# Optimization experiments

Hardware: AMD Instinct MI355X
Metric: run time of the kernel (lower is better)

The kernel has to match this reference:

```python
import jax, jax.numpy as jnp
import numpy as np

# Model constants (from Equilibrium3BConfig + hardcoded MambaBlock args)
D_MODEL = 2560
D_INNER = 5120          # expand=2
N_STATE = 128           # d_state
HEADS = 80              # d_inner // headdim
P_HEAD = 64             # headdim
D_CONV = 4
CONV_DIM = D_INNER + 2 * N_STATE        # 5376 (x, B, C share the conv)
D_IN_PROJ = 2 * D_INNER + 2 * N_STATE + HEADS  # 10576 (z, xBC, dt)
N_EXPERTS = 16
TOP_K = 2
M_INTER = 864
MS_INTER = 1728
EPS = 1e-6


def _rms(x, w, eps=EPS):
    xf = x.astype(jnp.float32)
    xf = xf * jax.lax.rsqrt(jnp.mean(xf * xf, axis=-1, keepdims=True) + eps)
    return w * xf.astype(x.dtype)


def setup_inputs() -> dict:
    key = jax.random.key(0)
    ks = jax.random.split(key, 16)
    b, l = 1, 1024
    s = 0.02  # weight scale, keeps activations sane through the deep block
    return {
        "hidden_states": jax.random.normal(ks[0], (b, l, D_MODEL), jnp.float32),
        "w_in": jax.random.normal(ks[1], (D_MODEL, D_IN_PROJ), jnp.float32) * s,
        "conv_w": jax.random.normal(ks[2], (CONV_DIM, D_CONV), jnp.float32) * s,
        "conv_b": jnp.zeros((CONV_DIM,), jnp.float32),
        "dt_bias": jax.random.normal(ks[3], (HEADS,), jnp.float32) * s,
        "A_log": jax.random.normal(ks[4], (HEADS,), jnp.float32) * s,
        "D": jnp.ones((HEADS,), jnp.float32),
        "mamba_norm_w": jnp.ones((D_INNER,), jnp.float32),
        "w_out": jax.random.normal(ks[5], (D_INNER, D_MODEL), jnp.float32) * s,
        "ln1_w": jnp.ones((D_MODEL,), jnp.float32),
        "ln2_w": jnp.ones((D_MODEL,), jnp.float32),
        "router_w": jax.random.normal(ks[6], (D_MODEL, N_EXPERTS), jnp.float32) * s,
        "we_gate": jax.random.normal(ks[7], (N_EXPERTS, D_MODEL, M_INTER), jnp.float32) * s,
        "we_up": jax.random.normal(ks[8], (N_EXPERTS, D_MODEL, M_INTER), jnp.float32) * s,
        "we_down": jax.random.normal(ks[9], (N_EXPERTS, M_INTER, D_MODEL), jnp.float32) * s,
        "ws_gate": jax.random.normal(ks[10], (D_MODEL, MS_INTER), jnp.float32) * s,
        "ws_up": jax.random.normal(ks[11], (D_MODEL, MS_INTER), jnp.float32) * s,
        "ws_down": jax.random.normal(ks[12], (MS_INTER, D_MODEL), jnp.float32) * s,
    }


def _forward(hidden_states, w_in, conv_w, conv_b, dt_bias, A_log, D, mamba_norm_w,
             w_out, ln1_w, ln2_w, router_w, we_gate, we_up, we_down,
             ws_gate, ws_up, ws_down):
    b, l, d = hidden_states.shape

    # ---- Mamba2 (selective scan) sub-block ----
    residual = hidden_states
    x = _rms(hidden_states, ln1_w)
    zxbcdt = x @ w_in  # [b, l, 10576]
    z, xBC, dt = jnp.split(zxbcdt, [D_INNER, D_INNER + CONV_DIM], axis=-1)

    # depthwise causal conv over (x, B, C) channels, then SiLU
    xBC_t = xBC.transpose(0, 2, 1)  # [b, c, l]
    conv = jax.lax.conv_general_dilated(
        xBC_t, conv_w[:, None, :], (1,), [(D_CONV - 1, 0)],
        feature_group_count=CONV_DIM, dimension_numbers=("NCH", "OIH", "NCH"))
    xBC = jax.nn.silu((conv + conv_b[None, :, None]).transpose(0, 2, 1))
    xs, Bc, Cc = jnp.split(xBC, [D_INNER, D_INNER + N_STATE], axis=-1)

    dt = jax.nn.softplus(dt + dt_bias)          # [b, l, h]
    A = -jnp.exp(A_log)                          # [h]
    xh = xs.reshape(b, l, HEADS, P_HEAD)

    # time-major for scan
    dt_l = dt.transpose(1, 0, 2)                 # [l, b, h]
    xh_l = xh.transpose(1, 0, 2, 3)              # [l, b, h, p]
    B_l = Bc.transpose(1, 0, 2)                  # [l, b, n]
    C_l = Cc.transpose(1, 0, 2)                  # [l, b, n]

    def step(h, inp):
        dt_t, x_t, B_t, C_t = inp
        dA = jnp.exp(dt_t * A)                   # [b, h]
        h = h * dA[..., None, None] + (dt_t[..., None] * x_t)[..., None] * B_t[:, None, None, :]
        y = jnp.einsum("bhpn,bn->bhp", h, C_t)
        return h, y

    h0 = jnp.zeros((b, HEADS, P_HEAD, N_STATE), hidden_states.dtype)
    _, y_l = jax.lax.scan(step, h0, (dt_l, xh_l, B_l, C_l))
    y_l = y_l + D[None, None, :, None] * xh_l    # skip term
    y = y_l.transpose(1, 0, 2, 3).reshape(b, l, D_INNER)
    y = _rms(y * jax.nn.silu(z), mamba_norm_w)   # gated RMSNorm
    hidden = residual + y @ w_out

    # ---- DeepSeekMoE sub-block ----
    residual2 = hidden
    xm = _rms(hidden, ln2_w).reshape(b * l, d)
    logits = xm @ router_w
    probs = jax.nn.softmax(logits.astype(jnp.float32), axis=-1)
    topv, topi = jax.lax.top_k(probs, TOP_K)
    topv = topv / jnp.sum(topv, axis=-1, keepdims=True)  # renormalize top-k
    wdense = jnp.sum(jax.nn.one_hot(topi, N_EXPERTS, dtype=xm.dtype)
                     * topv[..., None].astype(xm.dtype), axis=1)  # [T, E]

    # routed experts (SwiGLU), dense-masked faithful math
    hexp = (jax.nn.silu(jnp.einsum("td,edm->tem", xm, we_gate))
            * jnp.einsum("td,edm->tem", xm, we_up))
    y_routed = jnp.einsum("tem,emd,te->td", hexp, we_down, wdense)

    # shared experts (single fused SwiGLU MLP)
    y_shared = (jax.nn.silu(xm @ ws_gate) * (xm @ ws_up)) @ ws_down

    moe = (y_routed + y_shared).reshape(b, l, d)
    return residual2 + moe


def reference(hidden_states, w_in, conv_w, conv_b, dt_bias, A_log, D, mamba_norm_w,
              w_out, ln1_w, ln2_w, router_w, we_gate, we_up, we_down,
              ws_gate, ws_up, ws_down):
    return _forward(hidden_states, w_in, conv_w, conv_b, dt_bias, A_log, D,
                    mamba_norm_w, w_out, ln1_w, ln2_w, router_w,
                    we_gate, we_up, we_down, ws_gate, ws_up, ws_down)
```

## Files before the change

### kernel.cpp

```cpp
#include <hip/hip_runtime.h>

typedef __attribute__((ext_vector_type(4))) float f32x4;
typedef __attribute__((ext_vector_type(8))) __bf16 bf16x8;
typedef __attribute__((ext_vector_type(4))) __bf16 bf16x4;
typedef __attribute__((ext_vector_type(8))) _Float16 f16x8;
typedef __attribute__((ext_vector_type(4))) _Float16 f16x4;

#define D_MODEL 2560
#define D_INNER 5120
#define N_STATE 128
#define HEADS 80
#define P_HEAD 64
#define CONV_DIM 5376
#define D_INPROJ 10576
#define SEQ 1024
#define NCHUNK 16
#define QCHUNK 64
#define NEXP 16
#define M_INTER 864
#define MS_INTER 1728
#define NSLOT 2048
#define NSLOTP 2176

__device__ __forceinline__ float siluf(float x) { return x / (1.f + __expf(-x)); }

__device__ __forceinline__ int swz_p(int k4, int P) {
  return (k4 & ~31) | ((((k4 >> 3) & 3) ^ P) << 3) | (k4 & 7);
}

__device__ __forceinline__ void gl16(const __bf16* g, __bf16* l) {
  __builtin_amdgcn_global_load_lds((const __attribute__((address_space(1))) unsigned int*)g,
                                   (__attribute__((address_space(3))) unsigned int*)l, 16, 0, 0);
}

__device__ __forceinline__ float block_sum256(float v, float* red) {
#pragma unroll
  for (int m = 32; m > 0; m >>= 1) v += __shfl_xor(v, m, 64);
  int w = threadIdx.x >> 6;
  if ((threadIdx.x & 63) == 0) red[w] = v;
  __syncthreads();
  return red[0] + red[1] + red[2] + red[3];
}

template <bool FP16>
__global__ __launch_bounds__(256) void k_rmsnorm_p(const float* __restrict__ in,
                                                   const float* __restrict__ w,
                                                   float* __restrict__ f32out,
                                                   __bf16* __restrict__ ph,
                                                   __bf16* __restrict__ pdh,
                                                   __bf16* __restrict__ pdl, int D) {
  __shared__ float red[4];
  int t = blockIdx.x, tid = threadIdx.x;
  const float* x = in + (size_t)t * D;
  int nd4 = D >> 2;
  float ss = 0.f;
  for (int i = tid; i < nd4; i += 256) {
    float4 v = ((const float4*)x)[i];
    ss += v.x * v.x + v.y * v.y + v.z * v.z + v.w * v.w;
  }
  float tot = block_sum256(ss, red);
  float r = rsqrtf(tot / (float)D + 1e-6f);
  int P = (t >> 1) & 3;
  for (int i = tid; i < nd4; i += 256) {
    float4 v = ((const float4*)x)[i];
    float4 wv = ((const float4*)w)[i];
    float4 o;
    o.x = wv.x * v.x * r; o.y = wv.y * v.y * r; o.z = wv.z * v.z * r; o.w = wv.w * v.w * r;
    if (f32out) ((float4*)(f32out + (size_t)t * D))[i] = o;
    int p = swz_p(i * 4, P);
    if constexpr (FP16) {
      f16x4 hv;
      hv[0] = (_Float16)o.x; hv[1] = (_Float16)o.y; hv[2] = (_Float16)o.z; hv[3] = (_Float16)o.w;
      *(f16x4*)&ph[(size_t)t * D + p] = hv;
    } else {
      bf16x4 hv;
      hv[0] = (__bf16)o.x; hv[1] = (__bf16)o.y; hv[2] = (__bf16)o.z; hv[3] = (__bf16)o.w;
      *(bf16x4*)&ph[(size_t)t * D + p] = hv;
    }
    if (pdh) {
      int pp = swz_p(i * 4, P);
      bf16x4 hv, lv;
      hv[0] = (__bf16)o.x; hv[1] = (__bf16)o.y; hv[2] = (__bf16)o.z; hv[3] = (__bf16)o.w;
      lv[0] = (__bf16)(o.x - (float)hv[0]); lv[1] = (__bf16)(o.y - (float)hv[1]);
      lv[2] = (__bf16)(o.z - (float)hv[2]); lv[3] = (__bf16)(o.w - (float)hv[3]);
      *(bf16x4*)&pdh[(size_t)t * D + pp] = hv;
      *(bf16x4*)&pdl[(size_t)t * D + pp] = lv;
    }
  }
}

__global__ __launch_bounds__(256) void k_redrms(const float* __restrict__ Pp,
                                                const float* __restrict__ res,
                                                float* __restrict__ hidden,
                                                const float* __restrict__ w,
                                                float* __restrict__ f32out,
                                                __bf16* __restrict__ ph) {
  __shared__ float vbuf[D_MODEL];
  __shared__ float red[4];
  int t = blockIdx.x, tid = threadIdx.x;
  const int n4 = D_MODEL / 4;
  float ss = 0.f;
  for (int i = tid; i < n4; i += 256) {
    f32x4 a = *(const f32x4*)&res[(size_t)t * D_MODEL + i * 4];
#pragma unroll
    for (int z = 0; z < 4; z++)
      a += *(const f32x4*)&Pp[(size_t)z * SEQ * D_MODEL + (size_t)t * D_MODEL + i * 4];
    *(f32x4*)&vbuf[i * 4] = a;
    *(f32x4*)&hidden[(size_t)t * D_MODEL + i * 4] = a;
    ss += a[0] * a[0] + a[1] * a[1] + a[2] * a[2] + a[3] * a[3];
  }
  float tot = block_sum256(ss, red);
  float r = rsqrtf(tot / (float)D_MODEL + 1e-6f);
  int P = (t >> 1) & 3;
  for (int i = tid; i < n4; i += 256) {
    f32x4 v = *(const f32x4*)&vbuf[i * 4];
    float4 wv = *(const float4*)&w[i * 4];
    f32x4 o;
    o[0] = wv.x * v[0] * r; o[1] = wv.y * v[1] * r; o[2] = wv.z * v[2] * r; o[3] = wv.w * v[3] * r;
    *(f32x4*)&f32out[(size_t)t * D_MODEL + i * 4] = o;
    int p = swz_p(i * 4, P);
    bf16x4 hv;
    hv[0] = (__bf16)o[0]; hv[1] = (__bf16)o[1]; hv[2] = (__bf16)o[2]; hv[3] = (__bf16)o[3];
    *(bf16x4*)&ph[(size_t)t * D_MODEL + p] = hv;
  }
}

template <bool SPLIT, bool FP16>
__global__ __launch_bounds__(256) void k_transW(const float* __restrict__ W, int ld, int K, int N,
                                                __bf16* __restrict__ Th, __bf16* __restrict__ Tl) {
  __shared__ float T[64][65];
  const int n0 = blockIdx.x * 64, k0 = blockIdx.y * 64, tid = threadIdx.x;
#pragma unroll
  for (int i = 0; i < 16; i++) {
    int idx = tid + i * 256;
    int k = idx >> 6, n = idx & 63;
    float v = 0.f;
    if (n0 + n < N) v = W[(size_t)(k0 + k) * ld + n0 + n];
    T[k][n] = v;
  }
  __syncthreads();
#pragma unroll
  for (int i = 0; i < 4; i++) {
    int idx = tid + i * 256;
    int n = idx >> 4, p4 = (idx & 15) * 4;
    int nn = n0 + n;
    int P = (nn >> 1) & 3;
    if constexpr (SPLIT) {
      bf16x4 hv, lv;
#pragma unroll
      for (int e = 0; e < 4; e++) {
        int p = p4 + e;
        int kk = swz_p(p, P);
        float v = T[kk][n];
        __bf16 h = (__bf16)v;
        hv[e] = h;
        lv[e] = (__bf16)(v - (float)h);
      }
      *(bf16x4*)&Th[(size_t)nn * K + k0 + p4] = hv;
      *(bf16x4*)&Tl[(size_t)nn * K + k0 + p4] = lv;
    } else if constexpr (FP16) {
      f16x4 hv;
#pragma unroll
      for (int e = 0; e < 4; e++) {
        int p = p4 + e;
        int kk = swz_p(p, P);
        hv[e] = (_Float16)T[kk][n];
      }
      *(f16x4*)&Th[(size_t)nn * K + k0 + p4] = hv;
    } else {
      bf16x4 hv;
#pragma unroll
      for (int e = 0; e < 4; e++) {
        int p = p4 + e;
        int kk = swz_p(p, P);
        hv[e] = (__bf16)T[kk][n];
      }
      *(bf16x4*)&Th[(size_t)nn * K + k0 + p4] = hv;
    }
  }
}

template <bool SPLIT, bool FP16, bool PIPE>
__global__ __launch_bounds__(256) void k_gemm2(const __bf16* __restrict__ Ah,
                                               const __bf16* __restrict__ Al,
                                               const __bf16* __restrict__ Bh,
                                               const __bf16* __restrict__ Bl,
                                               float* __restrict__ C,
                                               int M, int N, int K, int ks, int nst) {
  constexpr int PLE = 4096;
  constexpr int NPL = SPLIT ? 4 : 2;
  constexpr int NBUF = PIPE ? 2 : 1;
  __shared__ __bf16 lds[NBUF * NPL * PLE];

  const int tid = threadIdx.x;
  const int T = gridDim.x * gridDim.y * gridDim.z;
  const int linear = blockIdx.x + gridDim.x * (blockIdx.y + gridDim.y * blockIdx.z);
  const int s_idx = (linear & 7) * (T >> 3) + (linear >> 3);
  const int bm = s_idx & 7;
  const int g = s_idx >> 3;
  const int bn = g % gridDim.y;
  const int z = g / gridDim.y;

  const int m0 = bm * 128, n0 = bn * 128;
  const int s0 = (int)(((long long)z * nst) / ks);
  const int s1 = (int)(((long long)(z + 1) * nst) / ks);
  float* __restrict__ Cp = C + (size_t)z * M * N;

  const int lane = tid & 63, wid = tid >> 6;
  const int wr = wid >> 1, wc = wid & 1;
  const int l16 = lane & 15, kl = lane >> 4;

  const int srow = tid >> 2;
  const int schunk = (tid & 3) * 8;
  const size_t aB0 = (size_t)(m0 + srow) * K + schunk;
  const size_t aB1 = aB0 + (size_t)64 * K;
  const size_t bB0 = (size_t)(n0 + srow) * K + schunk;
  const size_t bB1 = bB0 + (size_t)64 * K;

  int aoff[4], boff[4];
#pragma unroll
  for (int mi = 0; mi < 4; mi++) {
    int ra = wr * 64 + mi * 16 + l16;
    int rb = wc * 64 + mi * 16 + l16;
    aoff[mi] = ra * 64 + ((kl ^ ((ra >> 1) & 3)) << 4);
    boff[mi] = rb * 64 + ((kl ^ ((rb >> 1) & 3)) << 4);
  }

  f32x4 acc[4][4];
#pragma unroll
  for (int mi = 0; mi < 4; mi++)
#pragma unroll
    for (int ni = 0; ni < 4; ni++) acc[mi][ni] = f32x4{0.f, 0.f, 0.f, 0.f};

  auto STAGE = [&](int b, int kof) {
    __bf16* L = lds + (size_t)b * NPL * PLE;
    gl16(Ah + aB0 + kof, L + tid * 8);
    gl16(Ah + aB1 + kof, L + (tid + 256) * 8);
    gl16(Bh + bB0 + kof, L + (SPLIT ? 2 : 1) * PLE + tid * 8);
    gl16(Bh + bB1 + kof, L + (SPLIT ? 2 : 1) * PLE + (tid + 256) * 8);
    if constexpr (SPLIT) {
      gl16(Al + aB0 + kof, L + PLE + tid * 8);
      gl16(Al + aB1 + kof, L + PLE + (tid + 256) * 8);
      gl16(Bl + bB0 + kof, L + 3 * PLE + tid * 8);
      gl16(Bl + bB1 + kof, L + 3 * PLE + (tid + 256) * 8);
    }
  };

  auto COMPUTE = [&](const __bf16* L) {
    const char* AsH = (const char*)L;
    const char* BsH = (const char*)(L + (SPLIT ? 2 : 1) * PLE);
    if constexpr (!SPLIT && FP16) {
      f16x8 ah[4], bh[4];
#pragma unroll
      for (int mi = 0; mi < 4; mi++) ah[mi] = *(const f16x8*)(AsH + aoff[mi]);
#pragma unroll
      for (int ni = 0; ni < 4; ni++) bh[ni] = *(const f16x8*)(BsH + boff[ni]);
#pragma unroll
      for (int mi = 0; mi < 4; mi++)
#pragma unroll
        for (int ni = 0; ni < 4; ni++)
          acc[mi][ni] = __builtin_amdgcn_mfma_f32_16x16x32_f16(ah[mi], bh[ni], acc[mi][ni], 0, 0, 0);
    } else {
      bf16x8 ah[4], bh[4];
#pragma unroll
      for (int mi = 0; mi < 4; mi++) ah[mi] = *(const bf16x8*)(AsH + aoff[mi]);
#pragma unroll
      for (int ni = 0; ni < 4; ni++) bh[ni] = *(const bf16x8*)(BsH + boff[ni]);
#pragma unroll
      for (int mi = 0; mi < 4; mi++)
#pragma unroll
        for (int ni = 0; ni < 4; ni++)
          acc[mi][ni] = __builtin_amdgcn_mfma_f32_16x16x32_bf16(ah[mi], bh[ni], acc[mi][ni], 0, 0, 0);
      if constexpr (SPLIT) {
        const char* AsL = (const char*)(L + PLE);
        const char* BsL = (const char*)(L + 3 * PLE);
        bf16x8 al[4], bl[4];
#pragma unroll
        for (int mi = 0; mi < 4; mi++) al[mi] = *(const bf16x8*)(AsL + aoff[mi]);
#pragma unroll
        for (int ni = 0; ni < 4; ni++) bl[ni] = *(const bf16x8*)(BsL + boff[ni]);
#pragma unroll
        for (int mi = 0; mi < 4; mi++)
#pragma unroll
          for (int ni = 0; ni < 4; ni++) {
            acc[mi][ni] = __builtin_amdgcn_mfma_f32_16x16x32_bf16(ah[mi], bl[ni], acc[mi][ni], 0, 0, 0);
            acc[mi][ni] = __builtin_amdgcn_mfma_f32_16x16x32_bf16(al[mi], bh[ni], acc[mi][ni], 0, 0, 0);
          }
      }
    }
  };

  if constexpr (PIPE) {
    STAGE(0, s0 * 32);
    __syncthreads();
    int cur = 0;
    for (int s = s0; s < s1; ++s) {
      if (s + 1 < s1) STAGE(cur ^ 1, (s + 1) * 32);
      COMPUTE(lds + (size_t)cur * NPL * PLE);
      __syncthreads();
      cur ^= 1;
    }
  } else {
    for (int s = s0; s < s1; ++s) {
      __syncthreads();
      STAGE(0, s * 32);
      __syncthreads();
      COMPUTE(lds);
    }
  }

#pragma unroll
  for (int mi = 0; mi < 4; mi++)
#pragma unroll
    for (int ni = 0; ni < 4; ni++)
#pragma unroll
      for (int r = 0; r < 4; r++) {
        int row = m0 + wr * 64 + mi * 16 + kl * 4 + r;
        int col = n0 + wc * 64 + ni * 16 + l16;
        if (col < N) Cp[(size_t)row * N + col] = acc[mi][ni][r];
      }
}

__global__ void k_reduce(const float* __restrict__ Pp, int np, int n4, float* __restrict__ out) {
  int i = blockIdx.x * 256 + threadIdx.x;
  int stride = gridDim.x * 256;
  for (; i < n4; i += stride) {
    float4 a = ((const float4*)Pp)[i];
    for (int z = 1; z < np; z++) {
      float4 b = ((const float4*)Pp)[(size_t)z * n4 + i];
      a.x += b.x; a.y += b.y; a.z += b.z; a.w += b.w;
    }
    ((float4*)out)[i] = a;
  }
}

__global__ void k_dtfin(const float* __restrict__ dtP, const float* __restrict__ dt_bias,
                        const float* __restrict__ A_log, float* __restrict__ dtp,
                        float* __restrict__ dtA) {
  int t = blockIdx.x, h = threadIdx.x;
  if (h < HEADS) {
    float v = dt_bias[h];
#pragma unroll
    for (int z = 0; z < 8; z++) v += dtP[((size_t)z * SEQ + t) * 80 + h];
    float sp = fmaxf(v, 0.f) + log1pf(expf(-fabsf(v)));
    dtp[t * HEADS + h] = sp;
    dtA[t * HEADS + h] = sp * (-expf(A_log[h]));
  }
}

__global__ __launch_bounds__(256) void k_gatherA(const float* __restrict__ xm,
                                                 const int* __restrict__ perm,
                                                 __bf16* __restrict__ Aslots) {
  int s = blockIdx.x, tid = threadIdx.x;
  int t = perm[s];
  int P = (s >> 1) & 3;
  const float* src = xm + (size_t)t * D_MODEL;
  __bf16* dst = Aslots + (size_t)s * D_MODEL;
  for (int i = tid; i < D_MODEL / 4; i += 256) {
    float4 v = ((const float4*)src)[i];
    int p = swz_p(i * 4, P);
    bf16x4 h;
    h[0] = (__bf16)v.x; h[1] = (__bf16)v.y; h[2] = (__bf16)v.z; h[3] = (__bf16)v.w;
    *(bf16x4*)&dst[p] = h;
  }
}

template <int KS, int MS, bool DUAL>
__global__ __launch_bounds__(256) void k_gemmE2(const __bf16* __restrict__ Aall,
                                                const float* __restrict__ Bg,
                                                const float* __restrict__ Bg2,
                                                float* __restrict__ Cp,
                                                float* __restrict__ Cp2,
                                                const int* __restrict__ expOff,
                                                const int* __restrict__ expCnt,
                                                int N, int K, long long strideB, int bnHalf) {
  __shared__ __bf16 Asl[2][128 * 32];
  __shared__ __bf16 Bsl[2][128][40];
  const int tid = threadIdx.x;
  const int nbn = gridDim.x;
  const int T = gridDim.x * gridDim.y * gridDim.z;
  const int lin = blockIdx.x + gridDim.x * (blockIdx.y + gridDim.y * blockIdx.z);
  const int s_rm = (lin & 7) * (T >> 3) + (lin >> 3);
  const int chunk = T >> 3;
  const int xcd = s_rm / chunk;
  const int cpos = s_rm % chunk;
  const int gsub = cpos / nbn;
  int bn = cpos % nbn;
  const int grp = xcd + 8 * gsub;
  const int sub = grp % (KS * MS);
  const int ks = sub % KS;
  const int mh = sub / KS;
  const int e = grp / (KS * MS);

  const int cnt = expCnt[e], base = expOff[e];
  if (cnt == 0) return;
  const float* Bp = Bg;
  float* Cdst = Cp;
  if constexpr (DUAL) {
    if (bn >= bnHalf) {
      bn -= bnHalf;
      Bp = Bg2;
      Cdst = Cp2;
    }
  }
  Bp += (long long)e * strideB;
  const int n0 = bn * 128;
  const int nSteps = K / 32;
  const int st0 = (ks * nSteps) / KS;
  const int st1 = ((ks + 1) * nSteps) / KS;
  const int kBeg = st0 * 32;
  const int nIter = st1 - st0;
  float* __restrict__ Cpl = Cdst + (size_t)ks * NSLOTP * N;
  const int lane = tid & 63, wid = tid >> 6;
  const int wr = wid >> 1, wc = wid & 1;
  const int l16 = lane & 15, kl = lane >> 4;
  const int kb = tid >> 5, cb = tid & 31;
  const int arow = tid >> 2, achk = (tid & 3) * 8;
  const bool bok = (n0 + cb * 4) < N;

  const int cbl = cb & 3;
  int wrow[4];
#pragma unroll
  for (int e4 = 0; e4 < 4; e4++) wrow[e4] = cb * 4 + (e4 ^ cbl);

  int boffs[4];
#pragma unroll
  for (int ni = 0; ni < 4; ni++) {
    int col = wc * 64 + ni * 16 + l16;
    int prow = (col & ~3) | ((col & 3) ^ ((col >> 2) & 3));
    boffs[ni] = prow * 40 + kl * 8;
  }

  for (int bm = mh; bm * 128 < cnt; bm += MS) {
    const int rbase = base + bm * 128;
    int aoff[4];
#pragma unroll
    for (int mi = 0; mi < 4; mi++) {
      int r = wr * 64 + mi * 16 + l16;
      int P = ((rbase + r) >> 1) & 3;
      aoff[mi] = r * 64 + ((kl ^ P) << 4);
    }
    f32x4 acc[4][4];
#pragma unroll
    for (int mi = 0; mi < 4; mi++)
#pragma unroll
      for (int ni = 0; ni < 4; ni++) acc[mi][ni] = f32x4{0.f, 0.f, 0.f, 0.f};

    const size_t aBase = (size_t)(rbase + arow) * K + achk + kBeg;
    const size_t aBase2 = aBase + (size_t)64 * K;

    gl16(Aall + aBase, &Asl[0][tid * 8]);
    gl16(Aall + aBase2, &Asl[0][(tid + 256) * 8]);
    {
      const float* src = Bp + (size_t)(kBeg + kb * 4) * N + n0 + cb * 4;
      f32x4 bv[4];
#pragma unroll
      for (int j = 0; j < 4; j++)
        bv[j] = bok ? *(const f32x4*)(src + (size_t)j * N) : f32x4{0.f, 0.f, 0.f, 0.f};
#pragma unroll
      for (int e4 = 0; e4 < 4; e4++) {
        bf16x4 h;
        h[0] = (__bf16)bv[0][e4]; h[1] = (__bf16)bv[1][e4];
        h[2] = (__bf16)bv[2][e4]; h[3] = (__bf16)bv[3][e4];
        *(bf16x4*)&Bsl[0][wrow[e4]][kb * 4] = h;
      }
    }
    __syncthreads();
    int cur = 0;
    for (int kt = 0; kt < nIter; ++kt) {
      const bool more = (kt + 1 < nIter);
      f32x4 nv[4];
      if (more) {
        const int kOff = (kt + 1) * 32;
        gl16(Aall + aBase + kOff, &Asl[cur ^ 1][tid * 8]);
        gl16(Aall + aBase2 + kOff, &Asl[cur ^ 1][(tid + 256) * 8]);
        const float* src = Bp + (size_t)(kBeg + kOff + kb * 4) * N + n0 + cb * 4;
#pragma unroll
        for (int j = 0; j < 4; j++)
          nv[j] = bok ? *(const f32x4*)(src + (size_t)j * N) : f32x4{0.f, 0.f, 0.f, 0.f};
      }
      bf16x8 ah[4], bh[4];
#pragma unroll
      for (int mi = 0; mi < 4; mi++) ah[mi] = *(const bf16x8*)((const char*)&Asl[cur][0] + aoff[mi]);
#pragma unroll
      for (int ni = 0; ni < 4; ni++) bh[ni] = *(const bf16x8*)&Bsl[cur][0][boffs[ni]];
#pragma unroll
      for (int mi = 0; mi < 4; mi++)
#pragma unroll
        for (int ni = 0; ni < 4; ni++)
          acc[mi][ni] = __builtin_amdgcn_mfma_f32_16x16x32_bf16(ah[mi], bh[ni], acc[mi][ni], 0, 0, 0);
      if (more) {
#pragma unroll
        for (int e4 = 0; e4 < 4; e4++) {
          bf16x4 h;
          h[0] = (__bf16)nv[0][e4]; h[1] = (__bf16)nv[1][e4];
          h[2] = (__bf16)nv[2][e4]; h[3] = (__bf16)nv[3][e4];
          *(bf16x4*)&Bsl[cur ^ 1][wrow[e4]][kb * 4] = h;
        }
      }
      __syncthreads();
      cur ^= 1;
    }
#pragma unroll
    for (int mi = 0; mi < 4; mi++)
#pragma unroll
      for (int ni = 0; ni < 4; ni++)
#pragma unroll
        for (int r = 0; r < 4; r++) {
          int rl = bm * 128 + wr * 64 + mi * 16 + kl * 4 + r;
          int col = n0 + wc * 64 + ni * 16 + l16;
          if (rl < cnt && col < N) Cpl[(size_t)(base + rl) * N + col] = acc[mi][ni][r];
        }
  }
}

__global__ __launch_bounds__(256) void k_silumulE(const float* __restrict__ gP,
                                                  const float* __restrict__ uP,
                                                  const float* __restrict__ slotw,
                                                  __bf16* __restrict__ outp) {
  int s = blockIdx.x, tid = threadIdx.x;
  float w = slotw[s];
  int P = (s >> 1) & 3;
  const size_t PL = (size_t)NSLOTP * M_INTER;
  for (int i = tid; i < M_INTER / 4; i += 256) {
    f32x4 g = f32x4{0.f, 0.f, 0.f, 0.f}, u = f32x4{0.f, 0.f, 0.f, 0.f};
#pragma unroll
    for (int z = 0; z < 4; z++) {
      g += *(const f32x4*)&gP[z * PL + (size_t)s * M_INTER + i * 4];
      u += *(const f32x4*)&uP[z * PL + (size_t)s * M_INTER + i * 4];
    }
    int p = swz_p(i * 4, P);
    bf16x4 h;
    h[0] = (__bf16)(siluf(g[0]) * u[0] * w);
    h[1] = (__bf16)(siluf(g[1]) * u[1] * w);
    h[2] = (__bf16)(siluf(g[2]) * u[2] * w);
    h[3] = (__bf16)(siluf(g[3]) * u[3] * w);
    *(bf16x4*)&outp[(size_t)s * M_INTER + p] = h;
  }
}

__global__ __launch_bounds__(256) void k_silumul_sh2(const float* __restrict__ P4,
                                                     __bf16* __restrict__ outp) {
  int t = blockIdx.x, tid = threadIdx.x;
  int P = (t >> 1) & 3;
  const size_t PL = (size_t)SEQ * 3456;
  for (int i = tid; i < MS_INTER / 4; i += 256) {
    f32x4 g = f32x4{0.f, 0.f, 0.f, 0.f}, u = f32x4{0.f, 0.f, 0.f, 0.f};
#pragma unroll
    for (int z = 0; z < 4; z++) {
      g += *(const f32x4*)&P4[z * PL + (size_t)t * 3456 + i * 4];
      u += *(const f32x4*)&P4[z * PL + (size_t)t * 3456 + 1728 + i * 4];
    }
    int p = swz_p(i * 4, P);
    bf16x4 h;
    h[0] = (__bf16)(siluf(g[0]) * u[0]);
    h[1] = (__bf16)(siluf(g[1]) * u[1]);
    h[2] = (__bf16)(siluf(g[2]) * u[2]);
    h[3] = (__bf16)(siluf(g[3]) * u[3]);
    *(bf16x4*)&outp[(size_t)t * MS_INTER + p] = h;
  }
}

__global__ void k_conv(const float* __restrict__ zx, const float* __restrict__ cw,
                       const float* __restrict__ cb, float* __restrict__ xBC) {
  int cidx = blockIdx.x * 256 + threadIdx.x;
  int t = blockIdx.y;
  if (cidx < CONV_DIM) {
    float acc = cb[cidx];
#pragma unroll
    for (int j = 0; j < 4; j++) {
      int tt = t - 3 + j;
      if (tt >= 0) acc += zx[(size_t)tt * D_INPROJ + D_INNER + cidx] * cw[cidx * 4 + j];
    }
    xBC[(size_t)t * CONV_DIM + cidx] = siluf(acc);
  }
}

__global__ __launch_bounds__(256) void k_scan_intra(
    const float* __restrict__ xBC, const float* __restrict__ dtp,
    const float* __restrict__ dtA, float* __restrict__ y, float* __restrict__ S,
    float* __restrict__ cumA, float* __restrict__ Atot) {
  __shared__ float Bs[64 * 128];
  __shared__ float CG[64 * 128];
  __shared__ _Float16 Xs[64 * 64];
  __shared__ float da_s[64], a_s[64], dt_sh[64], w_sh[64];
  int c = blockIdx.x, h = blockIdx.y, tid = threadIdx.x;
  int t0 = c * QCHUNK;
#pragma unroll
  for (int i = 0; i < 8; i++) {
    int id = tid + 256 * i;
    int r = id >> 5, nc = id & 31;
    int sc = (nc ^ ((r >> 2) & 7)) * 4;
    *(float4*)&Bs[r * 128 + sc] = *(const float4*)&xBC[(size_t)(t0 + r) * CONV_DIM + D_INNER + nc * 4];
    *(float4*)&CG[r * 128 + sc] = *(const float4*)&xBC[(size_t)(t0 + r) * CONV_DIM + D_INNER + N_STATE + nc * 4];
  }
#pragma unroll
  for (int i = 0; i < 4; i++) {
    int id = tid + 256 * i;
    int r = id >> 4, p4 = (id & 15) * 4;
    float4 v = *(const float4*)&xBC[(size_t)(t0 + r) * CONV_DIM + h * P_HEAD + p4];
    f16x4 hv;
    hv[0] = (_Float16)v.x; hv[1] = (_Float16)v.y; hv[2] = (_Float16)v.z; hv[3] = (_Float16)v.w;
    *(f16x4*)&Xs[r * 64 + p4] = hv;
  }
  if (tid < 64) {
    da_s[tid] = dtA[(size_t)(t0 + tid) * HEADS + h];
    dt_sh[tid] = dtp[(size_t)(t0 + tid) * HEADS + h];
  }
  __syncthreads();
  if (tid < 64) {
    float a = 0.f;
    for (int i = 0; i <= tid; i++) a += da_s[i];
    a_s[tid] = a;
    cumA[((size_t)c * HEADS + h) * QCHUNK + tid] = a;
  }
  __syncthreads();
  if (tid < 64) {
    w_sh[tid] = __expf(a_s[63] - a_s[tid]) * dt_sh[tid];
    if (tid == 0) Atot[c * HEADS + h] = a_s[63];
  }
  __syncthreads();
  float gacc[4][4];
  {
    int tq = tid >> 4, sq = tid & 15;
#pragma unroll
    for (int j = 0; j < 4; j++)
#pragma unroll
      for (int jj = 0; jj < 4; jj++) gacc[j][jj] = 0.f;
    for (int nc = 0; nc < 32; nc++) {
      float4 cv[4], bv[4];
#pragma unroll
      for (int j = 0; j < 4; j++) {
        int rt = tq * 4 + j;
        cv[j] = *(const float4*)&CG[rt * 128 + ((nc ^ ((rt >> 2) & 7)) * 4)];
        int rs = sq * 4 + j;
        bv[j] = *(const float4*)&Bs[rs * 128 + ((nc ^ ((rs >> 2) & 7)) * 4)];
      }
#pragma unroll
      for (int j = 0; j < 4; j++)
#pragma unroll
        for (int jj = 0; jj < 4; jj++)
          gacc[j][jj] += cv[j].x * bv[jj].x + cv[j].y * bv[jj].y + cv[j].z * bv[jj].z + cv[j].w * bv[jj].w;
    }
  }
  __syncthreads();
  {
    int tq = tid >> 4, sq = tid & 15;
#pragma unroll
    for (int j = 0; j < 4; j++) {
      int t = tq * 4 + j;
      f32x4 gr;
#pragma unroll
      for (int jj = 0; jj < 4; jj++) {
        int s = sq * 4 + jj;
        float arg = fminf(a_s[t] - a_s[s], 0.f);
        gr[jj] = (s <= t) ? gacc[j][jj] * __expf(arg) * dt_sh[s] : 0.f;
      }
      *(f32x4*)&CG[t * 64 + ((sq ^ (t & 7)) * 4)] = gr;
    }
  }
  __syncthreads();
  {
    int tq = tid >> 4, pq = tid & 15;
    float4 acc[4];
#pragma unroll
    for (int j = 0; j < 4; j++) acc[j] = float4{0.f, 0.f, 0.f, 0.f};
    for (int s = 0; s < 64; s++) {
      f16x4 xh = *(const f16x4*)&Xs[s * 64 + pq * 4];
      float xv0 = (float)xh[0], xv1 = (float)xh[1], xv2 = (float)xh[2], xv3 = (float)xh[3];
#pragma unroll
      for (int j = 0; j < 4; j++) {
        int t = tq * 4 + j;
        float g = CG[t * 64 + (((s >> 2) ^ (t & 7)) * 4) + (s & 3)];
        acc[j].x += g * xv0; acc[j].y += g * xv1; acc[j].z += g * xv2; acc[j].w += g * xv3;
      }
    }
#pragma unroll
    for (int j = 0; j < 4; j++) {
      int t = tq * 4 + j;
      *(float4*)&y[(size_t)(t0 + t) * D_INNER + h * P_HEAD + pq * 4] = acc[j];
    }
  }
  {
    int p2 = tid >> 5, ncc = tid & 31;
    float4 acc[8];
#pragma unroll
    for (int j = 0; j < 8; j++) acc[j] = float4{0.f, 0.f, 0.f, 0.f};
    for (int s = 0; s < 64; s++) {
      float4 bvv = *(const float4*)&Bs[s * 128 + ((ncc ^ ((s >> 2) & 7)) * 4)];
      float ws = w_sh[s];
#pragma unroll
      for (int j = 0; j < 8; j++) {
        float xw = (float)Xs[s * 64 + p2 * 8 + j] * ws;
        acc[j].x += xw * bvv.x; acc[j].y += xw * bvv.y; acc[j].z += xw * bvv.z; acc[j].w += xw * bvv.w;
      }
    }
    size_t bb = ((size_t)(c * HEADS + h) * 64) * 128;
#pragma unroll
    for (int j = 0; j < 8; j++)
      *(float4*)&S[bb + (size_t)(p2 * 8 + j) * 128 + ncc * 4] = acc[j];
  }
}

__global__ void k_scan_state(float* __restrict__ S, const float* __restrict__ Atot) {
  int gid = blockIdx.x * 256 + threadIdx.x;
  int h = gid >> 13;
  int rem = gid & 8191;
  float run = 0.f;
#pragma unroll
  for (int c = 0; c < NCHUNK; c++) {
    size_t idx = ((size_t)(c * HEADS + h) << 13) + rem;
    float s = S[idx];
    S[idx] = run;
    run = run * __expf(Atot[c * HEADS + h]) + s;
  }
}

__global__ __launch_bounds__(256) void k_scan_inter(
    const float* __restrict__ xBC, const float* __restrict__ Hin,
    const float* __restrict__ cumA, const float* __restrict__ Dv,
    float* __restrict__ y) {
  __shared__ float Hs[64 * 128];
  __shared__ float Cs[64 * 128];
  __shared__ float a_l[64];
  int c = blockIdx.x, h = blockIdx.y, tid = threadIdx.x;
  int t0 = c * QCHUNK;
#pragma unroll
  for (int i = 0; i < 8; i++) {
    int id = tid + 256 * i;
    int r = id >> 5, nc = id & 31;
    int sc = (nc ^ ((r >> 2) & 7)) * 4;
    *(float4*)&Hs[r * 128 + sc] = *(const float4*)&Hin[(((size_t)(c * HEADS + h) * 64 + r) << 7) + nc * 4];
    *(float4*)&Cs[r * 128 + sc] = *(const float4*)&xBC[(size_t)(t0 + r) * CONV_DIM + D_INNER + N_STATE + nc * 4];
  }
  if (tid < 64) a_l[tid] = cumA[((size_t)c * HEADS + h) * QCHUNK + tid];
  __syncthreads();
  float Dh = Dv[h];
  int tq = tid >> 4, pq = tid & 15;
  float4 acc[4];
#pragma unroll
  for (int j = 0; j < 4; j++) acc[j] = float4{0.f, 0.f, 0.f, 0.f};
  for (int nc = 0; nc < 32; nc++) {
    float4 cv[4], hv[4];
#pragma unroll
    for (int j = 0; j < 4; j++) {
      int rt = tq * 4 + j;
      cv[j] = *(const float4*)&Cs[rt * 128 + ((nc ^ ((rt >> 2) & 7)) * 4)];
      int rp = pq * 4 + j;
      hv[j] = *(const float4*)&Hs[rp * 128 + ((nc ^ ((rp >> 2) & 7)) * 4)];
    }
#pragma unroll
    for (int j = 0; j < 4; j++) {
      acc[j].x += cv[j].x * hv[0].x + cv[j].y * hv[0].y + cv[j].z * hv[0].z + cv[j].w * hv[0].w;
      acc[j].y += cv[j].x * hv[1].x + cv[j].y * hv[1].y + cv[j].z * hv[1].z + cv[j].w * hv[1].w;
      acc[j].z += cv[j].x * hv[2].x + cv[j].y * hv[2].y + cv[j].z * hv[2].z + cv[j].w * hv[2].w;
      acc[j].w += cv[j].x * hv[3].x + cv[j].y * hv[3].y + cv[j].z * hv[3].z + cv[j].w * hv[3].w;
    }
  }
#pragma unroll
  for (int j = 0; j < 4; j++) {
    int t = tq * 4 + j;
    float e = __expf(a_l[t]);
    float4 xv = *(const float4*)&xBC[(size_t)(t0 + t) * CONV_DIM + h * P_HEAD + pq * 4];
    size_t yoff = (size_t)(t0 + t) * D_INNER + h * P_HEAD + pq * 4;
    float4 yv = *(float4*)&y[yoff];
    yv.x += e * acc[j].x + Dh * xv.x;
    yv.y += e * acc[j].y + Dh * xv.y;
    yv.z += e * acc[j].z + Dh * xv.z;
    yv.w += e * acc[j].w + Dh * xv.w;
    *(float4*)&y[yoff] = yv;
  }
}

__global__ __launch_bounds__(256) void k_gatednorm_p(const float* __restrict__ y,
                                                     const float* __restrict__ zx,
                                                     const float* __restrict__ w,
                                                     __bf16* __restrict__ ph) {
  __shared__ float vbuf[D_INNER];
  __shared__ float red[4];
  int t = blockIdx.x, tid = threadIdx.x;
  float ss = 0.f;
  for (int i = tid; i < D_INNER / 4; i += 256) {
    float4 yv = *(const float4*)&y[(size_t)t * D_INNER + i * 4];
    float4 zv = *(const float4*)&zx[(size_t)t * D_INPROJ + i * 4];
    float4 v;
    v.x = yv.x * siluf(zv.x); v.y = yv.y * siluf(zv.y);
    v.z = yv.z * siluf(zv.z); v.w = yv.w * siluf(zv.w);
    *(float4*)&vbuf[i * 4] = v;
    ss += v.x * v.x + v.y * v.y + v.z * v.z + v.w * v.w;
  }
  float tot = block_sum256(ss, red);
  float r = rsqrtf(tot / (float)D_INNER + 1e-6f);
  int P = (t >> 1) & 3;
  for (int i = tid; i < D_INNER / 4; i += 256) {
    float4 v = *(const float4*)&vbuf[i * 4];
    float4 wv = *(const float4*)&w[i * 4];
    float4 o;
    o.x = wv.x * v.x * r; o.y = wv.y * v.y * r; o.z = wv.z * v.z * r; o.w = wv.w * v.w * r;
    int p = swz_p(i * 4, P);
    f16x4 hv;
    hv[0] = (_Float16)o.x; hv[1] = (_Float16)o.y; hv[2] = (_Float16)o.z; hv[3] = (_Float16)o.w;
    *(f16x4*)&ph[(size_t)t * D_INNER + p] = hv;
  }
}

__global__ void k_zero(int* counts, int* cursor) {
  int i = threadIdx.x;
  if (i < NEXP) { counts[i] = 0; cursor[i] = 0; }
}

__global__ __launch_bounds__(256) void k_router(const float* __restrict__ xm,
                                                const float* __restrict__ Wr,
                                                int* __restrict__ top_i,
                                                float* __restrict__ top_v,
                                                int* __restrict__ counts) {
  __shared__ float part[16][17];
  __shared__ float lg[16];
  int t = blockIdx.x, tid = threadIdx.x;
  int e = tid & 15, seg = tid >> 4;
  const float* xr = xm + (size_t)t * D_MODEL;
  float s = 0.f;
  for (int i = 0; i < 160; i++) {
    int k = seg * 160 + i;
    s += xr[k] * Wr[(size_t)k * NEXP + e];
  }
  part[seg][e] = s;
  __syncthreads();
  if (tid < 16) {
    float l = 0.f;
    for (int g = 0; g < 16; g++) l += part[g][tid];
    lg[tid] = l;
  }
  __syncthreads();
  if (tid == 0) {
    float mx = lg[0];
    for (int i = 1; i < 16; i++) mx = fmaxf(mx, lg[i]);
    float pe[16];
    for (int i = 0; i < 16; i++) pe[i] = expf(lg[i] - mx);
    int i0 = 0; float v0 = pe[0];
    for (int i = 1; i < 16; i++) if (pe[i] > v0) { v0 = pe[i]; i0 = i; }
    int i1 = -1; float v1 = -1.f;
    for (int i = 0; i < 16; i++) if (i != i0 && pe[i] > v1) { v1 = pe[i]; i1 = i; }
    float inv = 1.f / (v0 + v1);
    top_i[t * 2] = i0; top_i[t * 2 + 1] = i1;
    top_v[t * 2] = v0 * inv; top_v[t * 2 + 1] = v1 * inv;
    atomicAdd(&counts[i0], 1);
    atomicAdd(&counts[i1], 1);
  }
}

__global__ void k_offsets(const int* counts, int* offs, int* cursor) {
  if (threadIdx.x == 0) {
    int s = 0;
    for (int e = 0; e < NEXP; e++) { offs[e] = s; cursor[e] = s; s += counts[e]; }
  }
}

__global__ void k_scatter(const int* __restrict__ top_i, const float* __restrict__ top_v,
                          int* __restrict__ cursor, int* __restrict__ perm,
                          int* __restrict__ slotOf, float* __restrict__ slotw) {
  int t = blockIdx.x * 256 + threadIdx.x;
  if (t < SEQ) {
    for (int k = 0; k < 2; k++) {
      int e = top_i[t * 2 + k];
      int pos = atomicAdd(&cursor[e], 1);
      perm[pos] = t;
      slotOf[t * 2 + k] = pos;
      slotw[pos] = top_v[t * 2 + k];
    }
  }
}

__global__ void k_final2(const float* __restrict__ hidden, const float* __restrict__ sh,
                         const float* __restrict__ dsP, const int* __restrict__ slotOf,
                         float* __restrict__ out) {
  int t = blockIdx.y;
  int d4 = (blockIdx.x * 256 + threadIdx.x) * 4;
  if (d4 < D_MODEL) {
    int s0 = slotOf[t * 2], s1 = slotOf[t * 2 + 1];
    f32x4 a = *(const f32x4*)&hidden[(size_t)t * D_MODEL + d4];
    f32x4 b = *(const f32x4*)&sh[(size_t)t * D_MODEL + d4];
    f32x4 acc = a + b;
    const size_t PL = (size_t)NSLOTP * D_MODEL;
#pragma unroll
    for (int z = 0; z < 3; z++) {
      acc += *(const f32x4*)&dsP[z * PL + (size_t)s0 * D_MODEL + d4];
      acc += *(const f32x4*)&dsP[z * PL + (size_t)s1 * D_MODEL + d4];
    }
    *(f32x4*)&out[(size_t)t * D_MODEL + d4] = acc;
  }
}

extern "C" void kernel_launch(void* const* d_in, const int* in_sizes, int n_in,
                              void* d_out, int out_size, void* d_ws, size_t ws_size,
                              hipStream_t stream) {
  const float* hs = (const float*)d_in[0];
  const float* w_in = (const float*)d_in[1];
  const float* conv_w = (const float*)d_in[2];
  const float* conv_b = (const float*)d_in[3];
  const float* dt_bias = (const float*)d_in[4];
  const float* A_log = (const float*)d_in[5];
  const float* Dv = (const float*)d_in[6];
  const float* mnw = (const float*)d_in[7];
  const float* w_out = (const float*)d_in[8];
  const float* ln1 = (const float*)d_in[9];
  const float* ln2 = (const float*)d_in[10];
  const float* router_w = (const float*)d_in[11];
  const float* we_gate = (const float*)d_in[12];
  const float* we_up = (const float*)d_in[13];
  const float* we_down = (const float*)d_in[14];
  const float* ws_gate = (const float*)d_in[15];
  const float* ws_up = (const float*)d_in[16];
  const float* ws_down = (const float*)d_in[17];

  char* base = (char*)d_ws;
  size_t off = 0;
  auto A = [&](size_t bytes) -> void* {
    void* p = base + off;
    off += (bytes + 255) & ~(size_t)255;
    return p;
  };
  float* xbc = (float*)A((size_t)SEQ * CONV_DIM * 4);
  float* xmf = (float*)A((size_t)SEQ * D_MODEL * 4);
  float* dtp = (float*)A((size_t)SEQ * HEADS * 4);
  float* dtA = (float*)A((size_t)SEQ * HEADS * 4);
  float* yf = (float*)A((size_t)SEQ * D_INNER * 4);
  float* cumA = (float*)A((size_t)NCHUNK * HEADS * QCHUNK * 4);
  float* Atot = (float*)A((size_t)NCHUNK * HEADS * 4);
  float* Sbuf = (float*)A((size_t)NCHUNK * HEADS * 64 * 128 * 4);
  float* hidden = (float*)A((size_t)SEQ * D_MODEL * 4);
  float* shout = (float*)A((size_t)SEQ * D_MODEL * 4);
  float* top_v = (float*)A(8192);
  float* slotw = (float*)A(8192);
  int* top_i = (int*)A(8192);
  int* counts = (int*)A(64);
  int* offs = (int*)A(64);
  int* cursor = (int*)A(64);
  int* perm = (int*)A(8192);
  int* slotOf = (int*)A(8192);
  __bf16* xp_h = (__bf16*)A((size_t)SEQ * D_MODEL * 2);
  __bf16* ybp_h = (__bf16*)A((size_t)SEQ * D_INNER * 2);
  __bf16* gbuf_bh = (__bf16*)A((size_t)SEQ * MS_INTER * 2);
  char* REG = (char*)A((size_t)163000000);

  __bf16* winT_h = (__bf16*)REG;
  float* zx = (float*)(REG + 60000000);
  float* partials = (float*)(REG + 104000000);
  __bf16* xdt_h = (__bf16*)(REG + 147000000);
  __bf16* xdt_l = (__bf16*)(REG + 152500000);
  __bf16* wdt_h = (__bf16*)(REG + 158000000);
  __bf16* wdt_l = (__bf16*)(REG + 158700000);
  float* dtP = (float*)(REG + 159400000);
  __bf16* woutT_h = (__bf16*)REG;
  __bf16* guT = (__bf16*)REG;
  __bf16* downT = (__bf16*)(REG + 18350080);
  float* partials4 = (float*)(REG + 30000000);
  __bf16* Aslots = (__bf16*)REG;
  __bf16* gsl = (__bf16*)(REG + 12000000);
  float* gateP = (float*)(REG + 16000000);
  float* upP = (float*)(REG + 77000000);
  float* dslotsP = (float*)(REG + 16000000);

  k_rmsnorm_p<true><<<SEQ, 256, 0, stream>>>(hs, ln1, nullptr, xp_h, xdt_h, xdt_l, D_MODEL);
  k_transW<false, true><<<dim3(166, 40), 256, 0, stream>>>(w_in, D_INPROJ, D_MODEL, D_INPROJ,
                                                           winT_h, nullptr);
  k_transW<true, false><<<dim3(2, 40), 256, 0, stream>>>(w_in + 10496, D_INPROJ, D_MODEL, 80,
                                                         wdt_h, wdt_l);
  k_gemm2<false, true, true><<<dim3(8, 83, 1), 256, 0, stream>>>(
      xp_h, nullptr, winT_h, nullptr, zx, SEQ, D_INPROJ, D_MODEL, 1, 80);
  k_gemm2<true, false, false><<<dim3(8, 1, 8), 256, 0, stream>>>(
      xdt_h, xdt_l, wdt_h, wdt_l, dtP, SEQ, 80, D_MODEL, 8, 80);
  k_dtfin<<<SEQ, 128, 0, stream>>>(dtP, dt_bias, A_log, dtp, dtA);
  k_conv<<<dim3(21, SEQ), 256, 0, stream>>>(zx, conv_w, conv_b, xbc);
  k_scan_intra<<<dim3(NCHUNK, HEADS), 256, 0, stream>>>(xbc, dtp, dtA, yf, Sbuf, cumA, Atot);
  k_scan_state<<<2560, 256, 0, stream>>>(Sbuf, Atot);
  k_scan_inter<<<dim3(NCHUNK, HEADS), 256, 0, stream>>>(xbc, Sbuf, cumA, Dv, yf);
  k_gatednorm_p<<<SEQ, 256, 0, stream>>>(yf, zx, mnw, ybp_h);
  k_transW<false, true><<<dim3(40, 80), 256, 0, stream>>>(w_out, D_MODEL, D_INNER, D_MODEL,
                                                          woutT_h, nullptr);
  k_gemm2<false, true, true><<<dim3(8, 20, 4), 256, 0, stream>>>(
      ybp_h, nullptr, woutT_h, nullptr, partials, SEQ, D_MODEL, D_INNER, 4, 160);
  k_redrms<<<SEQ, 256, 0, stream>>>(partials, hs, hidden, ln2, xmf, xp_h);

  k_zero<<<1, 64, 0, stream>>>(counts, cursor);
  k_router<<<SEQ, 256, 0, stream>>>(xmf, router_w, top_i, top_v, counts);
  k_offsets<<<1, 32, 0, stream>>>(counts, offs, cursor);
  k_scatter<<<4, 256, 0, stream>>>(top_i, top_v, cursor, perm, slotOf, slotw);

  k_transW<false, false><<<dim3(27, 40), 256, 0, stream>>>(ws_gate, MS_INTER, D_MODEL, MS_INTER,
                                                           guT, nullptr);
  k_transW<false, false><<<dim3(27, 40), 256, 0, stream>>>(ws_up, MS_INTER, D_MODEL, MS_INTER,
                                                           guT + (size_t)MS_INTER * D_MODEL, nullptr);
  k_gemm2<false, false, true><<<dim3(8, 27, 4), 256, 0, stream>>>(
      xp_h, nullptr, guT, nullptr, partials4, SEQ, 3456, D_MODEL, 4, 80);
  k_silumul_sh2<<<SEQ, 256, 0, stream>>>(partials4, gbuf_bh);
  k_transW<false, false><<<dim3(40, 27), 256, 0, stream>>>(ws_down, D_MODEL, MS_INTER, D_MODEL,
                                                           downT, nullptr);
  k_gemm2<false, false, true><<<dim3(8, 20, 4), 256, 0, stream>>>(
      gbuf_bh, nullptr, downT, nullptr, partials4, SEQ, D_MODEL, MS_INTER, 4, 54);
  k_reduce<<<2048, 256, 0, stream>>>(partials4, 4, SEQ * D_MODEL / 4, shout);

  k_gatherA<<<NSLOT, 256, 0, stream>>>(xmf, perm, Aslots);
  k_gemmE2<4, 2, true><<<dim3(14, 8, NEXP), 256, 0, stream>>>(
      Aslots, we_gate, we_up, gateP, upP, offs, counts,
      M_INTER, D_MODEL, (long long)D_MODEL * M_INTER, 7);
  k_silumulE<<<NSLOT, 256, 0, stream>>>(gateP, upP, slotw, gsl);
  k_gemmE2<3, 2, false><<<dim3(20, 6, NEXP), 256, 0, stream>>>(
      gsl, we_down, nullptr, dslotsP, nullptr, offs, counts,
      D_MODEL, M_INTER, (long long)M_INTER * D_MODEL, 0);

  k_final2<<<dim3(3, SEQ), 256, 0, stream>>>(hidden, shout, dslotsP, slotOf, (float*)d_out);
}
```

Measured before the change: 735.5 us.

## Remove LDS staging from expert GEMM and feed MFMA directly from global

The routed-expert GEMM no longer stages its A and B tiles through double-buffered shared memory with barriers. Each wave now loads its own A fragments straight from the pre-swizzled bf16 activations and gathers eight strided fp32 weight values per lane, converting them to bf16 in registers. This removes the LDS traffic, the swizzled stores and the per-step __syncthreads. In exchange, waves that share tiles load the same data again, the B gathers are narrow scalar strided reads, and there is no explicit prefetch to hide global latency.

```diff
diff --git a/kernel.cpp b/kernel.cpp
--- a/kernel.cpp
+++ b/kernel.cpp
@@ -374,8 +374,6 @@
                                                 const int* __restrict__ expOff,
                                                 const int* __restrict__ expCnt,
                                                 int N, int K, long long strideB, int bnHalf) {
-  __shared__ __bf16 Asl[2][128 * 32];
-  __shared__ __bf16 Bsl[2][128][40];
   const int tid = threadIdx.x;
   const int nbn = gridDim.x;
   const int T = gridDim.x * gridDim.y * gridDim.z;
@@ -414,31 +412,23 @@
   const int lane = tid & 63, wid = tid >> 6;
   const int wr = wid >> 1, wc = wid & 1;
   const int l16 = lane & 15, kl = lane >> 4;
-  const int kb = tid >> 5, cb = tid & 31;
-  const int arow = tid >> 2, achk = (tid & 3) * 8;
-  const bool bok = (n0 + cb * 4) < N;
-
-  const int cbl = cb & 3;
-  int wrow[4];
-#pragma unroll
-  for (int e4 = 0; e4 < 4; e4++) wrow[e4] = cb * 4 + (e4 ^ cbl);
-
-  int boffs[4];
+
+  const float* bptr[4];
 #pragma unroll
   for (int ni = 0; ni < 4; ni++) {
-    int col = wc * 64 + ni * 16 + l16;
-    int prow = (col & ~3) | ((col & 3) ^ ((col >> 2) & 3));
-    boffs[ni] = prow * 40 + kl * 8;
+    int c = n0 + wc * 64 + ni * 16 + l16;
+    if (c >= N) c = N - 1;
+    bptr[ni] = Bp + (size_t)(kBeg + kl * 8) * N + c;
   }
 
   for (int bm = mh; bm * 128 < cnt; bm += MS) {
     const int rbase = base + bm * 128;
-    int aoff[4];
+    const __bf16* aptr[4];
 #pragma unroll
     for (int mi = 0; mi < 4; mi++) {
-      int r = wr * 64 + mi * 16 + l16;
-      int P = ((rbase + r) >> 1) & 3;
-      aoff[mi] = r * 64 + ((kl ^ P) << 4);
+      int r = rbase + wr * 64 + mi * 16 + l16;
+      int P = (r >> 1) & 3;
+      aptr[mi] = Aall + (size_t)r * K + kBeg + ((kl ^ P) << 3);
     }
     f32x4 acc[4][4];
 #pragma unroll
@@ -446,61 +436,34 @@
 #pragma unroll
       for (int ni = 0; ni < 4; ni++) acc[mi][ni] = f32x4{0.f, 0.f, 0.f, 0.f};
 
-    const size_t aBase = (size_t)(rbase + arow) * K + achk + kBeg;
-    const size_t aBase2 = aBase + (size_t)64 * K;
-
-    gl16(Aall + aBase, &Asl[0][tid * 8]);
-    gl16(Aall + aBase2, &Asl[0][(tid + 256) * 8]);
-    {
-      const float* src = Bp + (size_t)(kBeg + kb * 4) * N + n0 + cb * 4;
-      f32x4 bv[4];
-#pragma unroll
-      for (int j = 0; j < 4; j++)
-        bv[j] = bok ? *(const f32x4*)(src + (size_t)j * N) : f32x4{0.f, 0.f, 0.f, 0.f};
-#pragma unroll
-      for (int e4 = 0; e4 < 4; e4++) {
-        bf16x4 h;
-        h[0] = (__bf16)bv[0][e4]; h[1] = (__bf16)bv[1][e4];
-        h[2] = (__bf16)bv[2][e4]; h[3] = (__bf16)bv[3][e4];
-        *(bf16x4*)&Bsl[0][wrow[e4]][kb * 4] = h;
+    for (int kt = 0; kt < nIter; ++kt) {
+      bf16x8 ah[4];
+#pragma unroll
+      for (int mi = 0; mi < 4; mi++) ah[mi] = *(const bf16x8*)(aptr[mi] + kt * 32);
+      bf16x8 bh[4];
+#pragma unroll
+      for (int ni = 0; ni < 4; ni++) {
+        const float* s = bptr[ni] + (size_t)kt * 32 * N;
+        float bv0 = s[0];
+        float bv1 = s[(size_t)N];
+        float bv2 = s[(size_t)2 * N];
+        float bv3 = s[(size_t)3 * N];
+        float bv4 = s[(size_t)4 * N];
+        float bv5 = s[(size_t)5 * N];
+        float bv6 = s[(size_t)6 * N];
+        float bv7 = s[(size_t)7 * N];
+        bf16x8 b;
+        b[0] = (__bf16)bv0; b[1] = (__bf16)bv1; b[2] = (__bf16)bv2; b[3] = (__bf16)bv3;
+        b[4] = (__bf16)bv4; b[5] = (__bf16)bv5; b[6] = (__bf16)bv6; b[7] = (__bf16)bv7;
+        bh[ni] = b;
       }
-    }
-    __syncthreads();
-    int cur = 0;
-    for (int kt = 0; kt < nIter; ++kt) {
-      const bool more = (kt + 1 < nIter);
-      f32x4 nv[4];
-      if (more) {
-        const int kOff = (kt + 1) * 32;
-        gl16(Aall + aBase + kOff, &Asl[cur ^ 1][tid * 8]);
-        gl16(Aall + aBase2 + kOff, &Asl[cur ^ 1][(tid + 256) * 8]);
-        const float* src = Bp + (size_t)(kBeg + kOff + kb * 4) * N + n0 + cb * 4;
-#pragma unroll
-        for (int j = 0; j < 4; j++)
-          nv[j] = bok ? *(const f32x4*)(src + (size_t)j * N) : f32x4{0.f, 0.f, 0.f, 0.f};
-      }
-      bf16x8 ah[4], bh[4];
-#pragma unroll
-      for (int mi = 0; mi < 4; mi++) ah[mi] = *(const bf16x8*)((const char*)&Asl[cur][0] + aoff[mi]);
-#pragma unroll
-      for (int ni = 0; ni < 4; ni++) bh[ni] = *(const bf16x8*)&Bsl[cur][0][boffs[ni]];
 #pragma unroll
       for (int mi = 0; mi < 4; mi++)
 #pragma unroll
         for (int ni = 0; ni < 4; ni++)
           acc[mi][ni] = __builtin_amdgcn_mfma_f32_16x16x32_bf16(ah[mi], bh[ni], acc[mi][ni], 0, 0, 0);
-      if (more) {
-#pragma unroll
-        for (int e4 = 0; e4 < 4; e4++) {
-          bf16x4 h;
-          h[0] = (__bf16)nv[0][e4]; h[1] = (__bf16)nv[1][e4];
-          h[2] = (__bf16)nv[2][e4]; h[3] = (__bf16)nv[3][e4];
-          *(bf16x4*)&Bsl[cur ^ 1][wrow[e4]][kb * 4] = h;
-        }
-      }
-      __syncthreads();
-      cur ^= 1;
-    }
+    }
+
 #pragma unroll
     for (int mi = 0; mi < 4; mi++)
 #pragma unroll
```

New measurement: 805.9 us. 9.6% more time.
